# Optimization experiments

Measured on AMD Instinct MI355X. Metric: run time of the kernel, lower is better.

The kernel has to match this reference:

```python
import jax, jax.numpy as jnp
import numpy as np

B, L, E = 8, 512, 256
H = W = 128
NH = 8
HD = E // NH


def setup_inputs() -> dict:
    key = jax.random.key(0)
    ks = jax.random.split(key, 8)
    return {
        "query_row": jax.random.normal(ks[0], (B, L, E), jnp.float32),
        "query_col": jax.random.normal(ks[1], (B, L, E), jnp.float32),
        "key_row": jax.random.normal(ks[2], (B, H, W, E), jnp.float32),
        "key_col": jax.random.normal(ks[3], (B, H, W, E), jnp.float32),
        "value": jax.random.normal(ks[4], (B, H, W, E), jnp.float32),
        "in_proj_weight": jax.random.normal(ks[5], (5 * E, E), jnp.float32) * 0.02,
        "in_proj_bias": jnp.zeros((5 * E,), jnp.float32),
        "out_proj_weight": jax.random.normal(ks[6], (E, E), jnp.float32) * 0.02,
        "out_proj_bias": jnp.zeros((E,), jnp.float32),
    }


def reference(query_row, query_col, key_row, key_col, value,
              in_proj_weight, in_proj_bias, out_proj_weight, out_proj_bias):
    b, tgt_len, embed_dim = query_row.shape
    h, w = key_col.shape[1], key_row.shape[2]
    nh, hd = NH, embed_dim // NH
    scale = float(hd) ** -0.5

    def proj(x, i):
        Wi = in_proj_weight[i * embed_dim:(i + 1) * embed_dim]
        bi = in_proj_bias[i * embed_dim:(i + 1) * embed_dim]
        return x @ Wi.T + bi

    q_row = proj(query_row, 0) * scale            # [B,L,E]
    q_col = proj(query_col, 1) * scale            # [B,L,E]
    k_row = proj(key_row, 2).mean(axis=1)         # mean over H -> [B,W,E]
    k_col = proj(key_col, 3).mean(axis=2)         # mean over W -> [B,H,E]
    v = proj(value, 4)                            # [B,H,W,E]

    def heads(x):  # [..., E] -> [B, nh, ..., hd]
        return x.reshape(x.shape[:-1] + (nh, hd))

    q_row_h = heads(q_row).transpose(0, 2, 1, 3)        # [B,nh,L,hd]
    q_col_h = heads(q_col).transpose(0, 2, 1, 3)        # [B,nh,L,hd]
    k_row_h = heads(k_row).transpose(0, 2, 1, 3)        # [B,nh,W,hd]
    k_col_h = heads(k_col).transpose(0, 2, 1, 3)        # [B,nh,H,hd]
    v_h = heads(v).transpose(0, 3, 1, 2, 4)             # [B,nh,H,W,hd]

    a_row = jax.nn.softmax(jnp.einsum('bnld,bnwd->bnlw', q_row_h, k_row_h), axis=-1)
    a_col = jax.nn.softmax(jnp.einsum('bnld,bnhd->bnlh', q_col_h, k_col_h), axis=-1)

    # contract over H first, then over W (matches torch's src_len_col >= src_len_row branch)
    ao_col = jnp.einsum('bnlh,bnhwc->bnlwc', a_col, v_h)      # [B,nh,L,W,hd]
    out = jnp.einsum('bnlw,bnlwc->bnlc', a_row, ao_col)       # [B,nh,L,hd]

    out = out.transpose(2, 0, 1, 3).reshape(tgt_len, b, embed_dim)  # [L,B,E]
    return out @ out_proj_weight.T + out_proj_bias
```

## Files before the change

kernel.cpp:

```cpp
#include <hip/hip_runtime.h>
#include <stdint.h>

#define B_  8
#define L_  512
#define E_  256
#define H_  128
#define W_  128
#define NH_ 8
#define HD_ 32

typedef unsigned short ushort_t;
typedef __attribute__((ext_vector_type(8))) short bf16x8;
typedef __attribute__((ext_vector_type(4))) float f32x4;

__device__ __forceinline__ float bf2f(ushort_t u) {
    union { unsigned int i; float f; } x;
    x.i = ((unsigned int)u) << 16;
    return x.f;
}
__device__ __forceinline__ ushort_t f2bf(float f) {
    union { float f; unsigned int i; } x;
    x.f = f;
    unsigned int r = x.i + 0x7FFFu + ((x.i >> 16) & 1u);
    return (ushort_t)(r >> 16);
}

__global__ __launch_bounds__(256) void mean_h_kernel(const float* __restrict__ kr,
                                                     float* __restrict__ out) {
    int i = blockIdx.x * 256 + threadIdx.x;
    int e = i & (E_ - 1);
    int w = (i >> 8) & (W_ - 1);
    int b = i >> 15;
    const float* p = kr + ((size_t)b * H_ * W_ + w) * E_ + e;
    float s = 0.f;
    for (int h = 0; h < H_; ++h) s += p[(size_t)h * W_ * E_];
    out[i] = s * (1.0f / H_);
}
__global__ __launch_bounds__(256) void mean_w_kernel(const float* __restrict__ kc,
                                                     float* __restrict__ out) {
    int i = blockIdx.x * 256 + threadIdx.x;
    int e = i & (E_ - 1);
    int h = (i >> 8) & (H_ - 1);
    int b = i >> 15;
    const float* p = kc + ((size_t)(b * H_ + h) * W_) * E_ + e;
    float s = 0.f;
    for (int w = 0; w < W_; ++w) s += p[(size_t)w * E_];
    out[i] = s * (1.0f / W_);
}

__device__ __forceinline__ void load4f(const float* p, float* v) {
    float4 t = *(const float4*)p;
    v[0] = t.x; v[1] = t.y; v[2] = t.z; v[3] = t.w;
}
__device__ __forceinline__ void store4(float* p, float a, float b, float c, float d) {
    float4 t; t.x = a; t.y = b; t.z = c; t.w = d;
    *(float4*)p = t;
}

__global__ __launch_bounds__(256) void gemm256(const float* __restrict__ A,
                                               const float* __restrict__ Wt,
                                               const float* __restrict__ bias,
                                               float* __restrict__ C, int M, float scale) {
    __shared__ __align__(16) float As[16][64];
    __shared__ __align__(16) float Bs[16][64];
    const int m0 = blockIdx.x * 64;
    const int n0 = blockIdx.y * 64;
    const int tid = threadIdx.x;
    const int lr = tid >> 2;
    const int lk = (tid & 3) << 2;
    const int tx = tid & 15, ty = tid >> 4;
    float acc[4][4] = {{0.f}};

    for (int k0 = 0; k0 < E_; k0 += 16) {
        float av[4], wv[4];
        load4f(A + (size_t)(m0 + lr) * E_ + k0 + lk, av);
        load4f(Wt + (size_t)(n0 + lr) * E_ + k0 + lk, wv);
        As[lk + 0][lr] = av[0]; As[lk + 1][lr] = av[1];
        As[lk + 2][lr] = av[2]; As[lk + 3][lr] = av[3];
        Bs[lk + 0][lr] = wv[0]; Bs[lk + 1][lr] = wv[1];
        Bs[lk + 2][lr] = wv[2]; Bs[lk + 3][lr] = wv[3];
        __syncthreads();
#pragma unroll
        for (int k = 0; k < 16; ++k) {
            float a[4], b[4];
            load4f(&As[k][ty << 2], a);
            load4f(&Bs[k][tx << 2], b);
#pragma unroll
            for (int i = 0; i < 4; ++i)
#pragma unroll
                for (int j = 0; j < 4; ++j) acc[i][j] += a[i] * b[j];
        }
        __syncthreads();
    }
    float bv[4];
    load4f(bias + n0 + (tx << 2), bv);
#pragma unroll
    for (int i = 0; i < 4; ++i) {
        float* cp = C + (size_t)(m0 + (ty << 2) + i) * E_ + n0 + (tx << 2);
        store4(cp, scale * (acc[i][0] + bv[0]), scale * (acc[i][1] + bv[1]),
                   scale * (acc[i][2] + bv[2]), scale * (acc[i][3] + bv[3]));
    }
}

__global__ __launch_bounds__(256) void wconv_kernel(const float* __restrict__ w,
                                                    ushort_t* __restrict__ wbf) {
    int i = (blockIdx.x * 256 + threadIdx.x) * 4;
    float4 f = *(const float4*)(w + i);
    ushort4 u;
    u.x = f2bf(f.x); u.y = f2bf(f.y); u.z = f2bf(f.z); u.w = f2bf(f.w);
    *(ushort4*)(wbf + i) = u;
}

#define KP_ 264
__global__ __launch_bounds__(256) void vproj_mfma(const float* __restrict__ Ag,
                                                  const ushort_t* __restrict__ Wbf,
                                                  const float* __restrict__ bias,
                                                  ushort_t* __restrict__ v_t) {
    __shared__ ushort_t A_lds[64 * KP_];
    const int m0 = blockIdx.x * 64;
    const int tid = threadIdx.x, lane = tid & 63, wv = tid >> 6;
    const int quad = lane >> 4, lc = lane & 15;
    {
        int r = tid >> 2, kq = (tid & 3) * 64;
        const float* sa = Ag + (size_t)(m0 + r) * 256 + kq;
        ushort_t* da = A_lds + r * KP_ + kq;
#pragma unroll
        for (int j = 0; j < 16; ++j) {
            float4 f = *(const float4*)(sa + j * 4);
            ushort4 u;
            u.x = f2bf(f.x); u.y = f2bf(f.y); u.z = f2bf(f.z); u.w = f2bf(f.w);
            *(ushort4*)(da + j * 4) = u;
        }
    }
    __syncthreads();
    bf16x8 bfr[8];
#pragma unroll
    for (int kc = 0; kc < 8; ++kc)
        bfr[kc] = *(const bf16x8*)(A_lds + (wv * 16 + lc) * KP_ + kc * 32 + quad * 8);

    const int b = m0 >> 14;
    const int ml = (m0 & 16383) + wv * 16 + lc;
    ushort_t* vtb = v_t + (size_t)b * 4194304 + ml;

    for (int g = 0; g < 4; ++g) {
        f32x4 acc[4];
#pragma unroll
        for (int t = 0; t < 4; ++t) { acc[t][0]=0.f; acc[t][1]=0.f; acc[t][2]=0.f; acc[t][3]=0.f; }
#pragma unroll
        for (int kc = 0; kc < 8; ++kc) {
#pragma unroll
            for (int t = 0; t < 4; ++t) {
                bf16x8 af = *(const bf16x8*)(Wbf + (size_t)(g * 64 + t * 16 + lc) * 256 + kc * 32 + quad * 8);
                acc[t] = __builtin_amdgcn_mfma_f32_16x16x32_bf16(af, bfr[kc], acc[t], 0, 0, 0);
            }
        }
#pragma unroll
        for (int t = 0; t < 4; ++t) {
            int e0 = g * 64 + t * 16 + quad * 4;
            float4 b4 = *(const float4*)(bias + e0);
            vtb[(size_t)(e0 + 0) * 16384] = f2bf(acc[t][0] + b4.x);
            vtb[(size_t)(e0 + 1) * 16384] = f2bf(acc[t][1] + b4.y);
            vtb[(size_t)(e0 + 2) * 16384] = f2bf(acc[t][2] + b4.z);
            vtb[(size_t)(e0 + 3) * 16384] = f2bf(acc[t][3] + b4.w);
        }
    }
}

__global__ __launch_bounds__(256) void scores_row(const float* __restrict__ q,
                                                  const float* __restrict__ k,
                                                  float* __restrict__ a) {
    const int lt = blockIdx.x, bn = blockIdx.y;
    const int n = bn & 7, b = bn >> 3;
    const int tid = threadIdx.x;
    __shared__ float ks[128][36];
    {
        int r = tid >> 1, c16 = (tid & 1) * 16;
        const float* src = k + ((size_t)b * 128 + r) * 256 + n * 32 + c16;
#pragma unroll
        for (int j = 0; j < 4; ++j) {
            float4 f = *(const float4*)(src + j * 4);
            ks[r][c16 + j * 4 + 0] = f.x; ks[r][c16 + j * 4 + 1] = f.y;
            ks[r][c16 + j * 4 + 2] = f.z; ks[r][c16 + j * 4 + 3] = f.w;
        }
    }
    const int ll = tid >> 3, wq = tid & 7;
    float4 q4r[8];
    {
        const float* qp = q + ((size_t)b * 512 + lt * 32 + ll) * 256 + n * 32;
#pragma unroll
        for (int c4 = 0; c4 < 8; ++c4) q4r[c4] = *(const float4*)(qp + c4 * 4);
    }
    __syncthreads();
    float dots[16];
#pragma unroll
    for (int j = 0; j < 16; ++j) dots[j] = 0.f;
#pragma unroll
    for (int c4 = 0; c4 < 8; ++c4) {
        float4 q4 = q4r[c4];
#pragma unroll
        for (int j = 0; j < 16; ++j) {
            float4 k4 = *(const float4*)&ks[j * 8 + wq][c4 * 4];
            dots[j] += q4.x * k4.x + q4.y * k4.y + q4.z * k4.z + q4.w * k4.w;
        }
    }
    float mx = dots[0];
#pragma unroll
    for (int j = 1; j < 16; ++j) mx = fmaxf(mx, dots[j]);
    for (int d = 1; d < 8; d <<= 1) mx = fmaxf(mx, __shfl_xor(mx, d, 64));
    float ex[16], sm = 0.f;
#pragma unroll
    for (int j = 0; j < 16; ++j) { ex[j] = __expf(dots[j] - mx); sm += ex[j]; }
    for (int d = 1; d < 8; d <<= 1) sm += __shfl_xor(sm, d, 64);
    float inv = 1.0f / sm;
    float* ap = a + ((size_t)bn * 512 + lt * 32 + ll) * 128 + wq;
#pragma unroll
    for (int j = 0; j < 16; ++j) ap[j * 8] = ex[j] * inv;
}

__global__ __launch_bounds__(256) void scores_col(const float* __restrict__ q,
                                                  const float* __restrict__ k,
                                                  float* __restrict__ ac_t) {
    const int lt = blockIdx.x, bn = blockIdx.y;
    const int n = bn & 7, b = bn >> 3;
    const int tid = threadIdx.x;
    __shared__ float qs[32][36];
    __shared__ float sc[128][33];
    __shared__ float mxr[8][32], smr[8][32], fin[2][32];
    {
        int r = tid >> 3, c4 = (tid & 7) * 4;
        float4 f = *(const float4*)(q + ((size_t)b * 512 + lt * 32 + r) * 256 + n * 32 + c4);
        qs[r][c4 + 0] = f.x; qs[r][c4 + 1] = f.y; qs[r][c4 + 2] = f.z; qs[r][c4 + 3] = f.w;
    }
    const int h = tid >> 1, lq = tid & 1;
    float4 kk[8];
    {
        const float* kp = k + ((size_t)b * 128 + h) * 256 + n * 32;
#pragma unroll
        for (int c4 = 0; c4 < 8; ++c4) kk[c4] = *(const float4*)(kp + c4 * 4);
    }
    __syncthreads();
    float dots[16];
#pragma unroll
    for (int j = 0; j < 16; ++j) dots[j] = 0.f;
#pragma unroll
    for (int c4 = 0; c4 < 8; ++c4) {
        float4 k4 = kk[c4];
#pragma unroll
        for (int j = 0; j < 16; ++j) {
            float4 q4 = *(const float4*)&qs[j * 2 + lq][c4 * 4];
            dots[j] += k4.x * q4.x + k4.y * q4.y + k4.z * q4.z + k4.w * q4.w;
        }
    }
#pragma unroll
    for (int j = 0; j < 16; ++j) sc[h][j * 2 + lq] = dots[j];
    __syncthreads();
    {
        int lcol = tid & 31, seg = tid >> 5;
        float m = -3.0e38f;
#pragma unroll
        for (int i = 0; i < 16; ++i) m = fmaxf(m, sc[seg * 16 + i][lcol]);
        mxr[seg][lcol] = m;
    }
    __syncthreads();
    if (tid < 32) {
        float m = mxr[0][tid];
#pragma unroll
        for (int s = 1; s < 8; ++s) m = fmaxf(m, mxr[s][tid]);
        fin[0][tid] = m;
    }
    __syncthreads();
    {
        int lcol = tid & 31, seg = tid >> 5;
        float m = fin[0][lcol], s = 0.f;
#pragma unroll
        for (int i = 0; i < 16; ++i) s += __expf(sc[seg * 16 + i][lcol] - m);
        smr[seg][lcol] = s;
    }
    __syncthreads();
    if (tid < 32) {
        float t = 0.f;
#pragma unroll
        for (int s = 1; s < 8; ++s) t += smr[s][tid];
        fin[1][tid] = 1.0f / (t + smr[0][tid]);
    }
    __syncthreads();
    {
        const int lh = (tid & 1) * 16;
        float* op = ac_t + ((size_t)bn * 128 + h) * 512 + lt * 32;
#pragma unroll
        for (int j4 = 0; j4 < 4; ++j4) {
            int l0 = lh + j4 * 4;
            float4 o;
            o.x = __expf(sc[h][l0 + 0] - fin[0][l0 + 0]) * fin[1][l0 + 0];
            o.y = __expf(sc[h][l0 + 1] - fin[0][l0 + 1]) * fin[1][l0 + 1];
            o.z = __expf(sc[h][l0 + 2] - fin[0][l0 + 2]) * fin[1][l0 + 2];
            o.w = __expf(sc[h][l0 + 3] - fin[0][l0 + 3]) * fin[1][l0 + 3];
            *(float4*)(op + l0) = o;
        }
    }
}

#define ARP 136
#define VBP 136
__global__ __launch_bounds__(256) void core_mfma(const float* __restrict__ a_row,
                                                 const float* __restrict__ ac_t,
                                                 const ushort_t* __restrict__ v_t,
                                                 float* __restrict__ attn) {
    __shared__ ushort_t ar_lds[64 * ARP];
    __shared__ ushort_t vb_lds[2][64 * VBP];
    const int blk = blockIdx.x;
    const int lt = blk >> 6, bn = blk & 63;
    const int n = bn & 7, b = bn >> 3;
    const int tid = threadIdx.x, lane = tid & 63, wv = tid >> 6;
    const int quad = lane >> 4, lc = lane & 15;

    {
        const size_t abase = ((size_t)bn * L_ + lt * 64) * 128;
        int r = tid >> 2, wq = (tid & 3) * 32;
        const float* src = a_row + abase + (size_t)r * 128 + wq;
        ushort_t* dst = ar_lds + r * ARP + wq;
#pragma unroll
        for (int j = 0; j < 8; ++j) {
            float4 f = *(const float4*)(src + j * 4);
            ushort4 u;
            u.x = f2bf(f.x); u.y = f2bf(f.y); u.z = f2bf(f.z); u.w = f2bf(f.w);
            *(ushort4*)(dst + j * 4) = u;
        }
    }
    const float* act = ac_t + (size_t)bn * 65536 + lt * 64 + wv * 16 + quad * 4;
    const ushort_t* vtb = v_t + (size_t)b * 4194304 + (size_t)(n * 32) * 16384;
    const int sc_ = tid >> 3, sw = (tid & 7) * 16;
#define STAGE2(hh, bu)                                                             \
    {                                                                              \
        const ushort_t* s0 = vtb + (size_t)sc_ * 16384 + (hh) * 128 + sw;          \
        ushort_t* d0 = vb_lds[bu] + sc_ * VBP + sw;                                \
        *(uint4*)d0 = *(const uint4*)s0;                                           \
        *(uint4*)(d0 + 8) = *(const uint4*)(s0 + 8);                               \
        const ushort_t* s1 = s0 + 128;                                             \
        ushort_t* d1 = d0 + 32 * VBP;                                              \
        *(uint4*)d1 = *(const uint4*)s1;                                           \
        *(uint4*)(d1 + 8) = *(const uint4*)(s1 + 8);                               \
    }
    STAGE2(0, 0);
    __syncthreads();
    bf16x8 A[4];
#pragma unroll
    for (int kc = 0; kc < 4; ++kc)
        A[kc] = *(const bf16x8*)(ar_lds + (wv * 16 + lc) * ARP + kc * 32 + quad * 8);

    f32x4 acc0 = {0.f,0.f,0.f,0.f}, acc1 = {0.f,0.f,0.f,0.f};
    for (int hh = 0; hh < 128; hh += 2) {
        const int buf = (hh >> 1) & 1;
        if (hh) __syncthreads();
        if (hh + 2 < 128) STAGE2(hh + 2, buf ^ 1);
        float4 av0 = *(const float4*)(act + (size_t)hh * 512);
        float4 av1 = *(const float4*)(act + (size_t)(hh + 1) * 512);
        const ushort_t* vb0 = vb_lds[buf];
        const ushort_t* vb1 = vb_lds[buf] + 32 * VBP;
        f32x4 t0 = {0.f,0.f,0.f,0.f}, t1 = {0.f,0.f,0.f,0.f};
        f32x4 u0 = {0.f,0.f,0.f,0.f}, u1 = {0.f,0.f,0.f,0.f};
#pragma unroll
        for (int kc = 0; kc < 4; ++kc) {
            const int ko = kc * 32 + quad * 8;
            bf16x8 b0 = *(const bf16x8*)(vb0 + lc * VBP + ko);
            bf16x8 b1 = *(const bf16x8*)(vb0 + (16 + lc) * VBP + ko);
            bf16x8 c0 = *(const bf16x8*)(vb1 + lc * VBP + ko);
            bf16x8 c1 = *(const bf16x8*)(vb1 + (16 + lc) * VBP + ko);
            t0 = __builtin_amdgcn_mfma_f32_16x16x32_bf16(A[kc], b0, t0, 0, 0, 0);
            t1 = __builtin_amdgcn_mfma_f32_16x16x32_bf16(A[kc], b1, t1, 0, 0, 0);
            u0 = __builtin_amdgcn_mfma_f32_16x16x32_bf16(A[kc], c0, u0, 0, 0, 0);
            u1 = __builtin_amdgcn_mfma_f32_16x16x32_bf16(A[kc], c1, u1, 0, 0, 0);
        }
        acc0[0] += av0.x * t0[0] + av1.x * u0[0]; acc1[0] += av0.x * t1[0] + av1.x * u1[0];
        acc0[1] += av0.y * t0[1] + av1.y * u0[1]; acc1[1] += av0.y * t1[1] + av1.y * u1[1];
        acc0[2] += av0.z * t0[2] + av1.z * u0[2]; acc1[2] += av0.z * t1[2] + av1.z * u1[2];
        acc0[3] += av0.w * t0[3] + av1.w * u0[3]; acc1[3] += av0.w * t1[3] + av1.w * u1[3];
    }
    const int row0 = wv * 16 + quad * 4;
#pragma unroll
    for (int r = 0; r < 4; ++r) {
        size_t o = ((size_t)(lt * 64 + row0 + r) * B_ + b) * E_ + n * HD_ + lc;
        attn[o] = acc0[r];
        attn[o + 16] = acc1[r];
    }
#undef STAGE2
}

extern "C" void kernel_launch(void* const* d_in, const int* in_sizes, int n_in,
                              void* d_out, int out_size, void* d_ws, size_t ws_size,
                              hipStream_t stream) {
    const float* query_row = (const float*)d_in[0];
    const float* query_col = (const float*)d_in[1];
    const float* key_row   = (const float*)d_in[2];
    const float* key_col   = (const float*)d_in[3];
    const float* value     = (const float*)d_in[4];
    const float* ipw       = (const float*)d_in[5];
    const float* ipb       = (const float*)d_in[6];
    const float* opw       = (const float*)d_in[7];
    const float* opb       = (const float*)d_in[8];
    float* out = (float*)d_out;

    char* ws = (char*)d_ws;
    float* q_row_s = (float*)ws;  ws += (size_t)4096 * 256 * 4;
    float* q_col_s = (float*)ws;  ws += (size_t)4096 * 256 * 4;
    float* krm     = (float*)ws;  ws += (size_t)262144 * 4;
    float* kcm     = (float*)ws;  ws += (size_t)262144 * 4;
    float* k_row   = (float*)ws;  ws += (size_t)262144 * 4;
    float* k_col   = (float*)ws;  ws += (size_t)262144 * 4;
    ushort_t* v_t  = (ushort_t*)ws; ws += (size_t)33554432 * 2;
    float* a_row   = (float*)ws;  ws += (size_t)4194304 * 4;
    float* ac_t    = (float*)ws;  ws += (size_t)4194304 * 4;
    float* attn    = (float*)ws;  ws += (size_t)4096 * 256 * 4;
    ushort_t* wbf  = (ushort_t*)ws; ws += (size_t)65536 * 2;

    const float scale = 0.17677669529663687f;

    mean_h_kernel<<<1024, 256, 0, stream>>>(key_row, krm);
    mean_w_kernel<<<1024, 256, 0, stream>>>(key_col, kcm);
    wconv_kernel<<<64, 256, 0, stream>>>(ipw + 4 * 65536, wbf);

    gemm256<<<dim3(64, 4), 256, 0, stream>>>(query_row, ipw + 0 * 65536, ipb + 0,    q_row_s, 4096, scale);
    gemm256<<<dim3(64, 4), 256, 0, stream>>>(query_col, ipw + 1 * 65536, ipb + 256,  q_col_s, 4096, scale);
    gemm256<<<dim3(16, 4), 256, 0, stream>>>(krm,       ipw + 2 * 65536, ipb + 512,  k_row,   1024, 1.0f);
    gemm256<<<dim3(16, 4), 256, 0, stream>>>(kcm,       ipw + 3 * 65536, ipb + 768,  k_col,   1024, 1.0f);

    vproj_mfma<<<2048, 256, 0, stream>>>(value, wbf, ipb + 1024, v_t);

    scores_row<<<dim3(16, 64), 256, 0, stream>>>(q_row_s, k_row, a_row);
    scores_col<<<dim3(16, 64), 256, 0, stream>>>(q_col_s, k_col, ac_t);

    core_mfma<<<512, 256, 0, stream>>>(a_row, ac_t, v_t, attn);

    gemm256<<<dim3(64, 4), 256, 0, stream>>>(attn, opw, opb, out, 4096, 1.0f);
}
```

Before: 690.1 us.

## Retile value projection so each wave owns 64 output features with vectorized stores

The value projection kernel now gives each wave a 64x64 tile (all 64 rows of the block by 64 output features) instead of 16 rows by all 256 features. Each loaded weight fragment is reused across four row tiles and each LDS activation fragment across four feature tiles, which cuts repeated global weight reads. Swapping MFMA operands puts the output transposed in registers, so the transposed v_t can be written with 8-byte ushort4 stores instead of scattered 2-byte stores. The cost is 64 accumulator registers per lane, which may lower occupancy.

```diff
diff --git a/kernel.cpp b/kernel.cpp
--- a/kernel.cpp
+++ b/kernel.cpp
@@ -133,35 +133,49 @@
         }
     }
     __syncthreads();
-    bf16x8 bfr[8];
-#pragma unroll
-    for (int kc = 0; kc < 8; ++kc)
-        bfr[kc] = *(const bf16x8*)(A_lds + (wv * 16 + lc) * KP_ + kc * 32 + quad * 8);
+
+    f32x4 acc[4][4];
+#pragma unroll
+    for (int t = 0; t < 4; ++t)
+#pragma unroll
+        for (int et = 0; et < 4; ++et) {
+            acc[t][et][0] = 0.f; acc[t][et][1] = 0.f;
+            acc[t][et][2] = 0.f; acc[t][et][3] = 0.f;
+        }
+
+    const ushort_t* wrow = Wbf + (size_t)(wv * 64 + lc) * 256 + quad * 8;
+
+#pragma unroll
+    for (int kc = 0; kc < 8; ++kc) {
+        bf16x8 vf[4];
+#pragma unroll
+        for (int t = 0; t < 4; ++t)
+            vf[t] = *(const bf16x8*)(A_lds + (t * 16 + lc) * KP_ + kc * 32 + quad * 8);
+#pragma unroll
+        for (int et = 0; et < 4; ++et) {
+            bf16x8 wf = *(const bf16x8*)(wrow + (size_t)(et * 16) * 256 + kc * 32);
+#pragma unroll
+            for (int t = 0; t < 4; ++t)
+                acc[t][et] = __builtin_amdgcn_mfma_f32_16x16x32_bf16(vf[t], wf, acc[t][et], 0, 0, 0);
+        }
+    }
 
     const int b = m0 >> 14;
-    const int ml = (m0 & 16383) + wv * 16 + lc;
-    ushort_t* vtb = v_t + (size_t)b * 4194304 + ml;
-
-    for (int g = 0; g < 4; ++g) {
-        f32x4 acc[4];
-#pragma unroll
-        for (int t = 0; t < 4; ++t) { acc[t][0]=0.f; acc[t][1]=0.f; acc[t][2]=0.f; acc[t][3]=0.f; }
-#pragma unroll
-        for (int kc = 0; kc < 8; ++kc) {
-#pragma unroll
-            for (int t = 0; t < 4; ++t) {
-                bf16x8 af = *(const bf16x8*)(Wbf + (size_t)(g * 64 + t * 16 + lc) * 256 + kc * 32 + quad * 8);
-                acc[t] = __builtin_amdgcn_mfma_f32_16x16x32_bf16(af, bfr[kc], acc[t], 0, 0, 0);
-            }
-        }
+    const int ml = m0 & 16383;
+    ushort_t* vtb = v_t + (size_t)b * 4194304 + ml + quad * 4;
+#pragma unroll
+    for (int et = 0; et < 4; ++et) {
+        const int e = wv * 64 + et * 16 + lc;
+        const float bv = bias[e];
+        ushort_t* vte = vtb + (size_t)e * 16384;
 #pragma unroll
         for (int t = 0; t < 4; ++t) {
-            int e0 = g * 64 + t * 16 + quad * 4;
-            float4 b4 = *(const float4*)(bias + e0);
-            vtb[(size_t)(e0 + 0) * 16384] = f2bf(acc[t][0] + b4.x);
-            vtb[(size_t)(e0 + 1) * 16384] = f2bf(acc[t][1] + b4.y);
-            vtb[(size_t)(e0 + 2) * 16384] = f2bf(acc[t][2] + b4.z);
-            vtb[(size_t)(e0 + 3) * 16384] = f2bf(acc[t][3] + b4.w);
+            ushort4 u;
+            u.x = f2bf(acc[t][et][0] + bv);
+            u.y = f2bf(acc[t][et][1] + bv);
+            u.z = f2bf(acc[t][et][2] + bv);
+            u.w = f2bf(acc[t][et][3] + bv);
+            *(ushort4*)(vte + t * 16) = u;
         }
     }
 }
```

Measured after the change: 618.1 us. 10.4% less time.
